# Performance work log

Measured on AMD Instinct MI355X. Metric: run time of the kernel, lower is better.

Reference implementation:

```python
import jax, jax.numpy as jnp
import numpy as np

B, D, F = 16384, 512, 28
GIN = D + D + F + 1  # 1053
EPS = 1e-5


def setup_inputs() -> dict:
    key = jax.random.key(0)
    ks = jax.random.split(key, 16)
    s = 0.02
    return {
        "team_embedding": jax.random.normal(ks[0], (B, D), jnp.float32),
        "opponent_embedding": jax.random.normal(ks[1], (B, D), jnp.float32),
        "game_features": jax.random.normal(ks[2], (B, F), jnp.float32),
        "won": jnp.round(jax.random.uniform(ks[3], (B, 1), jnp.float32)),
        # input_projection Linear(GIN -> D)
        "W_proj": jax.random.normal(ks[4], (D, GIN), jnp.float32) * s,
        "b_proj": jnp.zeros((D,), jnp.float32),
        # GRUCell params (PyTorch layout: [3D, *] with r,z,n blocks)
        "W_ih": jax.random.normal(ks[5], (3 * D, D), jnp.float32) * s,
        "b_ih": jnp.zeros((3 * D,), jnp.float32),
        "W_hh": jax.random.normal(ks[6], (3 * D, D), jnp.float32) * s,
        "b_hh": jnp.zeros((3 * D,), jnp.float32),
        # LayerNorm
        "gamma": jnp.ones((D,), jnp.float32),
        "beta": jnp.zeros((D,), jnp.float32),
        # game_importance MLP: D -> 128 -> 1
        "W_imp1": jax.random.normal(ks[7], (128, D), jnp.float32) * s,
        "b_imp1": jnp.zeros((128,), jnp.float32),
        "W_imp2": jax.random.normal(ks[8], (1, 128), jnp.float32) * s,
        "b_imp2": jnp.zeros((1,), jnp.float32),
    }


def reference(team_embedding, opponent_embedding, game_features, won,
              W_proj, b_proj, W_ih, b_ih, W_hh, b_hh,
              gamma, beta, W_imp1, b_imp1, W_imp2, b_imp2):
    # combined: [B, 2D+F+1]
    x = jnp.concatenate([team_embedding, opponent_embedding, game_features, won], axis=-1)
    # input_projection: Linear -> ReLU (Dropout is identity in eval)
    projected = jax.nn.relu(x @ W_proj.T + b_proj)  # [B, D]
    # game_importance: Linear -> ReLU -> Linear -> Sigmoid
    importance = jax.nn.sigmoid(jax.nn.relu(projected @ W_imp1.T + b_imp1) @ W_imp2.T + b_imp2)  # [B, 1]
    # GRUCell (PyTorch math)
    gi = projected @ W_ih.T + b_ih          # [B, 3D]
    gh = team_embedding @ W_hh.T + b_hh     # [B, 3D]
    i_r, i_z, i_n = jnp.split(gi, 3, axis=-1)
    h_r, h_z, h_n = jnp.split(gh, 3, axis=-1)
    r = jax.nn.sigmoid(i_r + h_r)
    z = jax.nn.sigmoid(i_z + h_z)
    n = jnp.tanh(i_n + r * h_n)
    new_embedding = (1.0 - z) * n + z * team_embedding
    # gated blend
    updated = team_embedding + importance * (new_embedding - team_embedding)
    # LayerNorm
    mu = jnp.mean(updated, axis=-1, keepdims=True)
    var = jnp.mean(jnp.square(updated - mu), axis=-1, keepdims=True)
    updated = gamma * (updated - mu) * jax.lax.rsqrt(var + EPS) + beta
    game_context = jax.lax.stop_gradient(projected)  # .detach().clone()
    return (updated, game_context)
```

## Files before the change

kernel.cpp:

```cpp
#include <hip/hip_runtime.h>
#include <hip/hip_bf16.h>


#define NB 16384
#define GINP 1088

typedef __bf16 bf16x8 __attribute__((ext_vector_type(8)));
typedef float f32x4 __attribute__((ext_vector_type(4)));
typedef unsigned short ushort8 __attribute__((ext_vector_type(8)));

__device__ __forceinline__ void gload_lds16(const void* g, void* l) {
  __builtin_amdgcn_global_load_lds(
      (const __attribute__((address_space(1))) void*)g,
      (__attribute__((address_space(3))) void*)l, 16, 0, 0);
}
__device__ __forceinline__ bf16x8 ds_read128(const unsigned short* l) {
  f32x4 r;
  asm volatile("ds_read_b128 %0, %1"
               : "=v"(r)
               : "v"((const __attribute__((address_space(3))) void*)l));
  bf16x8 out;
  __builtin_memcpy(&out, &r, 16);
  return out;
}
__device__ __forceinline__ float sigmoidf_(float x) { return 1.0f / (1.0f + expf(-x)); }
__device__ __forceinline__ float bf2f(unsigned short u) {
  unsigned int x = ((unsigned int)u) << 16;
  float f; __builtin_memcpy(&f, &x, 4); return f;
}

__global__ __launch_bounds__(256) void prep_x2(
    const float* __restrict__ team, const float* __restrict__ opp,
    const float* __restrict__ gf, const float* __restrict__ won,
    __hip_bfloat16* __restrict__ X) {
  long idx = (long)blockIdx.x * 256 + threadIdx.x;
  if (idx >= (long)NB * 136) return;
  const int r = (int)(idx / 136);
  const int c8 = (int)(idx % 136) * 8;
  float v[8];
  if (c8 < 512) {
    float4 a = *(const float4*)&team[(size_t)r * 512 + c8];
    float4 b = *(const float4*)&team[(size_t)r * 512 + c8 + 4];
    v[0]=a.x; v[1]=a.y; v[2]=a.z; v[3]=a.w; v[4]=b.x; v[5]=b.y; v[6]=b.z; v[7]=b.w;
  } else if (c8 < 1024) {
    float4 a = *(const float4*)&opp[(size_t)r * 512 + (c8 - 512)];
    float4 b = *(const float4*)&opp[(size_t)r * 512 + (c8 - 512) + 4];
    v[0]=a.x; v[1]=a.y; v[2]=a.z; v[3]=a.w; v[4]=b.x; v[5]=b.y; v[6]=b.z; v[7]=b.w;
  } else if (c8 < 1048) {
    const int g0 = c8 - 1024;
#pragma unroll
    for (int e = 0; e < 8; ++e) v[e] = gf[(size_t)r * 28 + g0 + e];
  } else if (c8 == 1048) {
    v[0] = gf[(size_t)r * 28 + 24]; v[1] = gf[(size_t)r * 28 + 25];
    v[2] = gf[(size_t)r * 28 + 26]; v[3] = gf[(size_t)r * 28 + 27];
    v[4] = won[r]; v[5] = 0.f; v[6] = 0.f; v[7] = 0.f;
  } else {
#pragma unroll
    for (int e = 0; e < 8; ++e) v[e] = 0.f;
  }
  __hip_bfloat16 h[8];
#pragma unroll
  for (int e = 0; e < 8; ++e) h[e] = __float2bfloat16(v[e]);
  *(uint4*)&X[(size_t)r * GINP + c8] = *(const uint4*)h;
}

__global__ __launch_bounds__(256) void prep_w2(
    const float* __restrict__ Wproj, const float* __restrict__ Wih,
    const float* __restrict__ Whh, const float* __restrict__ Wimp1,
    const float* __restrict__ bih, const float* __restrict__ bhh,
    __hip_bfloat16* __restrict__ Wpb, __hip_bfloat16* __restrict__ Wrz,
    __hip_bfloat16* __restrict__ Wn, __hip_bfloat16* __restrict__ Wimp1b,
    float* __restrict__ bcat) {
  long idx = (long)blockIdx.x * 256 + threadIdx.x;
  if (idx < 512L * 1088) {
    int r = (int)(idx / 1088), c = (int)(idx % 1088);
    Wpb[idx] = __float2bfloat16(c < 1053 ? Wproj[(size_t)r * 1053 + c] : 0.f);
    return;
  }
  idx -= 512L * 1088;
  if (idx < 1024L * 1024) {
    int q = (int)(idx >> 10), c = (int)(idx & 1023);
    float v = (c < 512) ? Wih[(size_t)q * 512 + c] : Whh[(size_t)q * 512 + (c - 512)];
    Wrz[idx] = __float2bfloat16(v);
    return;
  }
  idx -= 1024L * 1024;
  if (idx < 1024L * 512) {
    int q = (int)(idx / 512), c = (int)(idx % 512);
    float v = (q < 512) ? Wih[(size_t)(1024 + q) * 512 + c]
                        : Whh[(size_t)(1024 + q - 512) * 512 + c];
    Wn[idx] = __float2bfloat16(v);
    return;
  }
  idx -= 1024L * 512;
  if (idx < 128L * 512) { Wimp1b[idx] = __float2bfloat16(Wimp1[idx]); return; }
  idx -= 128L * 512;
  if (idx < 2048) {
    int j = (int)idx;
    float v;
    if (j < 1024) v = bih[j] + bhh[j];
    else if (j < 1536) v = bih[j];
    else v = bhh[j - 512];
    bcat[j] = v;
  }
}

__global__ __launch_bounds__(512, 1) void gemm_g8(
    const __hip_bfloat16* __restrict__ Pm, const __hip_bfloat16* __restrict__ Xb,
    const __hip_bfloat16* __restrict__ Wrz, const __hip_bfloat16* __restrict__ Wn,
    const float* __restrict__ bcat, __hip_bfloat16* __restrict__ gg) {
  __shared__ __align__(16) unsigned short ldsA[2 * 256 * 64];
  __shared__ __align__(16) unsigned short ldsB[2 * 256 * 64];

  const int tid = threadIdx.x;
  const int wid = tid >> 6, lane = tid & 63;
  const int wr = wid >> 2, wc = wid & 3;
  const int fl = lane & 15, kh = lane >> 4;
  const int srow = tid >> 3;
  const int sgp = tid & 7;

  const int tn = blockIdx.x & 7, tm = blockIdx.x >> 3;
  const int m0 = tm * 256;

  const __hip_bfloat16* Wp;
  int ldw, NT;
  if (tn < 4) { Wp = Wrz + (size_t)tn * 256 * 1024; ldw = 1024; NT = 16; }
  else        { Wp = Wn + (size_t)(tn - 4) * 256 * 512; ldw = 512; NT = 8; }
  const float* bp = bcat + tn * 256;

  auto stageA64 = [&](int s, int r0) {
    const __hip_bfloat16* Ap; int lda; int k0;
    if (tn < 4) {
      if (s < 8) { Ap = Pm; lda = 512; k0 = s * 64; }
      else       { Ap = Xb; lda = GINP; k0 = (s - 8) * 64; }
    } else if (tn < 6) { Ap = Pm; lda = 512; k0 = s * 64; }
    else               { Ap = Xb; lda = GINP; k0 = s * 64; }
    const int row = r0 + srow;
    const int gl = sgp ^ (row & 7);
    gload_lds16(Ap + (size_t)(m0 + row) * lda + k0 + gl * 8,
                &ldsA[(s & 1) * 16384 + (r0 + (wid << 3)) * 64]);
  };
  auto stageB64 = [&](int s, int r0) {
    const int row = r0 + srow;
    const int gl = sgp ^ (row & 7);
    gload_lds16(Wp + (size_t)row * ldw + s * 64 + gl * 8,
                &ldsB[(s & 1) * 16384 + (r0 + (wid << 3)) * 64]);
  };
  auto readA = [&](int sl, int m, int kk) -> bf16x8 {
    const int row = wr * 128 + m * 16 + fl;
    const int g = (kk * 4 + kh) ^ (row & 7);
    return ds_read128(&ldsA[sl + row * 64 + g * 8]);
  };
  auto readB = [&](int sl, int n, int kk) -> bf16x8 {
    const int row = wc * 64 + n * 16 + fl;
    const int g = (kk * 4 + kh) ^ (row & 7);
    return ds_read128(&ldsB[sl + row * 64 + g * 8]);
  };

  f32x4 acc[8][4];
#pragma unroll
  for (int m = 0; m < 8; ++m)
#pragma unroll
    for (int n = 0; n < 4; ++n) acc[m][n] = (f32x4){0.f, 0.f, 0.f, 0.f};

  stageA64(0, 0); stageA64(0, 64); stageA64(0, 128); stageA64(0, 192);
  stageB64(0, 0); stageB64(0, 64); stageB64(0, 128); stageB64(0, 192);
  stageA64(1, 0); stageA64(1, 64); stageA64(1, 128); stageA64(1, 192);
  stageB64(1, 0); stageB64(1, 64); stageB64(1, 128); stageB64(1, 192);
  asm volatile("s_waitcnt vmcnt(8)" ::: "memory");
  __builtin_amdgcn_s_barrier();

  for (int t = 0; t < NT; ++t) {
    const int sl = (t & 1) * 16384;
    const bool pf = (t + 2 < NT);
    bf16x8 fa0[4][2], fa1[4][2], fb0[2][2], fb1[2][2];

#pragma unroll
    for (int m = 0; m < 4; ++m) { fa0[m][0] = readA(sl, m, 0); fa0[m][1] = readA(sl, m, 1); }
#pragma unroll
    for (int n = 0; n < 2; ++n) { fb0[n][0] = readB(sl, n, 0); fb0[n][1] = readB(sl, n, 1); }
    __builtin_amdgcn_s_barrier();
    asm volatile("s_waitcnt lgkmcnt(0)" ::: "memory");
    __builtin_amdgcn_sched_barrier(0);
    __builtin_amdgcn_s_setprio(1);
#pragma unroll
    for (int kk = 0; kk < 2; ++kk)
#pragma unroll
      for (int m = 0; m < 4; ++m)
#pragma unroll
        for (int n = 0; n < 2; ++n)
          acc[m][n] = __builtin_amdgcn_mfma_f32_16x16x32_bf16(fa0[m][kk], fb0[n][kk], acc[m][n], 0, 0, 0);
    __builtin_amdgcn_s_setprio(0);
    __builtin_amdgcn_s_barrier();

#pragma unroll
    for (int m = 0; m < 4; ++m) { fa1[m][0] = readA(sl, m + 4, 0); fa1[m][1] = readA(sl, m + 4, 1); }
    if (pf) { stageA64(t + 2, 0); stageA64(t + 2, 128); }
    __builtin_amdgcn_s_barrier();
    asm volatile("s_waitcnt lgkmcnt(0)" ::: "memory");
    __builtin_amdgcn_sched_barrier(0);
    __builtin_amdgcn_s_setprio(1);
#pragma unroll
    for (int kk = 0; kk < 2; ++kk)
#pragma unroll
      for (int m = 0; m < 4; ++m)
#pragma unroll
        for (int n = 0; n < 2; ++n)
          acc[m + 4][n] = __builtin_amdgcn_mfma_f32_16x16x32_bf16(fa1[m][kk], fb0[n][kk], acc[m + 4][n], 0, 0, 0);
    __builtin_amdgcn_s_setprio(0);
    __builtin_amdgcn_s_barrier();

#pragma unroll
    for (int n = 0; n < 2; ++n) { fb1[n][0] = readB(sl, n + 2, 0); fb1[n][1] = readB(sl, n + 2, 1); }
    if (pf) { stageA64(t + 2, 64); stageA64(t + 2, 192); }
    __builtin_amdgcn_s_barrier();
    asm volatile("s_waitcnt lgkmcnt(0)" ::: "memory");
    __builtin_amdgcn_sched_barrier(0);
    __builtin_amdgcn_s_setprio(1);
#pragma unroll
    for (int kk = 0; kk < 2; ++kk)
#pragma unroll
      for (int m = 0; m < 4; ++m)
#pragma unroll
        for (int n = 0; n < 2; ++n)
          acc[m + 4][n + 2] = __builtin_amdgcn_mfma_f32_16x16x32_bf16(fa1[m][kk], fb1[n][kk], acc[m + 4][n + 2], 0, 0, 0);
    __builtin_amdgcn_s_setprio(0);
    __builtin_amdgcn_s_barrier();

    if (pf) { stageB64(t + 2, 0); stageB64(t + 2, 64); stageB64(t + 2, 128); stageB64(t + 2, 192); }
    __builtin_amdgcn_sched_barrier(0);
    __builtin_amdgcn_s_barrier();
    __builtin_amdgcn_s_setprio(1);
#pragma unroll
    for (int kk = 0; kk < 2; ++kk)
#pragma unroll
      for (int m = 0; m < 4; ++m)
#pragma unroll
        for (int n = 0; n < 2; ++n)
          acc[m][n + 2] = __builtin_amdgcn_mfma_f32_16x16x32_bf16(fa0[m][kk], fb1[n][kk], acc[m][n + 2], 0, 0, 0);
    __builtin_amdgcn_s_setprio(0);
    if (pf) { asm volatile("s_waitcnt vmcnt(8)" ::: "memory"); }
    else    { asm volatile("s_waitcnt vmcnt(0)" ::: "memory"); }
    __builtin_amdgcn_s_barrier();
  }

#pragma unroll
  for (int m = 0; m < 8; ++m)
#pragma unroll
    for (int n = 0; n < 4; ++n)
#pragma unroll
      for (int j = 0; j < 4; ++j) {
        const int lrow = wr * 128 + m * 16 + kh * 4 + j;
        const int lcol = wc * 64 + n * 16 + fl;
        gg[(size_t)(m0 + lrow) * 2048 + tn * 256 + lcol] =
            __float2bfloat16(acc[m][n][j] + bp[lcol]);
      }
}

template <int MODE>
__global__ __launch_bounds__(512, 1) void gemm_dp3(
    const __hip_bfloat16* __restrict__ A0, int lda0,
    const __hip_bfloat16* __restrict__ A1, int lda1,
    const __hip_bfloat16* __restrict__ W0, const __hip_bfloat16* __restrict__ W1,
    const float* __restrict__ bias,
    float* __restrict__ Cf, __hip_bfloat16* __restrict__ Cb,
    int tilesN, int NTP) {
  __shared__ __align__(16) unsigned short ldsA[3 * 256 * 64];
  __shared__ __align__(16) unsigned short ldsB[3 * 128 * 64];

  const int tid = threadIdx.x;
  const int wid = tid >> 6, lane = tid & 63;
  const int wr = wid >> 1, wc = wid & 1;
  const int fl = lane & 15, kh = lane >> 4;

  int bid = blockIdx.x;
  { const int cpx = gridDim.x >> 3; bid = (bid & 7) * cpx + (bid >> 3); }
  const int tm = bid / tilesN, tn = bid % tilesN;
  const int m0 = tm * 256;

  const __hip_bfloat16* Wp; int ldw, NT;
  Wp = W0 + (size_t)tn * 128 * GINP; ldw = GINP; NT = NTP;
  const float* bp = bias + tn * 128;

  const int prow_b = tid >> 3;
  const int gp = tid & 7;

  auto stageAB = [&](int s, int buf) {
    const int kW = s * 64;
    const __hip_bfloat16* Ap = A0; int lda = lda0; int kA = s * 64;
    unsigned short* la = &ldsA[buf * (256 * 64)];
    unsigned short* lb = &ldsB[buf * (128 * 64)];
#pragma unroll
    for (int i = 0; i < 4; ++i) {
      const int prow = i * 64 + prow_b;
      const int gl = gp ^ (prow & 7);
      gload_lds16(Ap + (size_t)(m0 + prow) * lda + kA + gl * 8,
                  la + i * 4096 + wid * 512);
    }
#pragma unroll
    for (int i = 0; i < 2; ++i) {
      const int prow = i * 64 + prow_b;
      const int gl = gp ^ (prow & 7);
      gload_lds16(Wp + (size_t)prow * ldw + kW + gl * 8,
                  lb + i * 4096 + wid * 512);
    }
  };

  f32x4 acc[4][4];
#pragma unroll
  for (int m = 0; m < 4; ++m)
#pragma unroll
    for (int n = 0; n < 4; ++n) acc[m][n] = (f32x4){0.f, 0.f, 0.f, 0.f};

  stageAB(0, 0);
  stageAB(1, 1);

  for (int t = 0; t < NT; ++t) {
    const int cur = t % 3;
    if (t + 1 < NT) { asm volatile("s_waitcnt vmcnt(6)" ::: "memory"); }
    else            { asm volatile("s_waitcnt vmcnt(0)" ::: "memory"); }
    __builtin_amdgcn_s_barrier();
    if (t + 2 < NT) stageAB(t + 2, (t + 2) % 3);

    const unsigned short* At = &ldsA[cur * (256 * 64)];
    const unsigned short* Bt = &ldsB[cur * (128 * 64)];
    bf16x8 af[2][4], bfr[2][4];
#pragma unroll
    for (int kk = 0; kk < 2; ++kk) {
#pragma unroll
      for (int m = 0; m < 4; ++m) {
        const int r = wr * 64 + m * 16 + fl;
        const int g = (kk * 4 + kh) ^ (r & 7);
        af[kk][m] = ds_read128(&At[r * 64 + g * 8]);
      }
#pragma unroll
      for (int n = 0; n < 4; ++n) {
        const int r = wc * 64 + n * 16 + fl;
        const int g = (kk * 4 + kh) ^ (r & 7);
        bfr[kk][n] = ds_read128(&Bt[r * 64 + g * 8]);
      }
    }
    asm volatile("s_waitcnt lgkmcnt(0)" ::: "memory");
    __builtin_amdgcn_sched_barrier(0);
    __builtin_amdgcn_s_setprio(1);
#pragma unroll
    for (int kk = 0; kk < 2; ++kk)
#pragma unroll
      for (int m = 0; m < 4; ++m)
#pragma unroll
        for (int n = 0; n < 4; ++n)
          acc[m][n] = __builtin_amdgcn_mfma_f32_16x16x32_bf16(af[kk][m], bfr[kk][n], acc[m][n], 0, 0, 0);
    __builtin_amdgcn_s_setprio(0);
  }

#pragma unroll
  for (int m = 0; m < 4; ++m)
#pragma unroll
    for (int n = 0; n < 4; ++n)
#pragma unroll
      for (int j = 0; j < 4; ++j) {
        const int lrow = wr * 64 + m * 16 + kh * 4 + j;
        const int lcol = wc * 64 + n * 16 + fl;
        const size_t grow = (size_t)(m0 + lrow);
        float v = acc[m][n][j] + bp[lcol];
        v = fmaxf(v, 0.f);
        Cf[grow * 512 + tn * 128 + lcol] = v;
        Cb[grow * 512 + tn * 128 + lcol] = __float2bfloat16(v);
      }
}

__global__ __launch_bounds__(256, 2) void gemm_imp2(
    const __hip_bfloat16* __restrict__ A, const __hip_bfloat16* __restrict__ W,
    const float* __restrict__ bias, const float* __restrict__ w2,
    const float* __restrict__ b2, float* __restrict__ imp) {
  __shared__ __align__(16) unsigned short ldsA[64 * 64];
  __shared__ __align__(16) unsigned short ldsB[128 * 64];
  __shared__ float sdot[64];
  const int tid = threadIdx.x;
  const int w = tid >> 6, lane = tid & 63;
  const int wr = w >> 1, wc = w & 1;
  const int fl = lane & 15, kh = lane >> 4;
  const int srow = lane >> 3, scol = (lane & 7) * 8;
  const int m0 = blockIdx.x * 64;

  if (tid < 64) sdot[tid] = 0.f;

  f32x4 acc[2][4];
#pragma unroll
  for (int m = 0; m < 2; ++m)
#pragma unroll
    for (int n = 0; n < 4; ++n) acc[m][n] = (f32x4){0.f, 0.f, 0.f, 0.f};

  for (int kt = 0; kt < 8; ++kt) {
    const int k0 = kt * 64;
#pragma unroll
    for (int c = 0; c < 2; ++c) {
      const int rgrp = c * 4 + w;
      const int row = rgrp * 8 + srow;
      gload_lds16(A + (size_t)(m0 + row) * 512 + k0 + scol, (char*)ldsA + rgrp * 1024);
    }
#pragma unroll
    for (int c = 0; c < 4; ++c) {
      const int rgrp = c * 4 + w;
      const int row = rgrp * 8 + srow;
      gload_lds16(W + (size_t)row * 512 + k0 + scol, (char*)ldsB + rgrp * 1024);
    }
    __syncthreads();
#pragma unroll
    for (int kk = 0; kk < 2; ++kk) {
      bf16x8 af[2], bfr[4];
#pragma unroll
      for (int m = 0; m < 2; ++m)
        af[m] = *(const bf16x8*)&ldsA[(wr * 32 + m * 16 + fl) * 64 + kk * 32 + kh * 8];
#pragma unroll
      for (int n = 0; n < 4; ++n)
        bfr[n] = *(const bf16x8*)&ldsB[(wc * 64 + n * 16 + fl) * 64 + kk * 32 + kh * 8];
#pragma unroll
      for (int m = 0; m < 2; ++m)
#pragma unroll
        for (int n = 0; n < 4; ++n)
          acc[m][n] = __builtin_amdgcn_mfma_f32_16x16x32_bf16(af[m], bfr[n], acc[m][n], 0, 0, 0);
    }
    __syncthreads();
  }
#pragma unroll
  for (int m = 0; m < 2; ++m)
#pragma unroll
    for (int j = 0; j < 4; ++j) {
      float p = 0.f;
#pragma unroll
      for (int n = 0; n < 4; ++n) {
        const int lcol = wc * 64 + n * 16 + fl;
        const float v = fmaxf(acc[m][n][j] + bias[lcol], 0.f);
        p += v * w2[lcol];
      }
      atomicAdd(&sdot[wr * 32 + m * 16 + kh * 4 + j], p);
    }
  __syncthreads();
  if (tid < 64) imp[m0 + tid] = sigmoidf_(sdot[tid] + b2[0]);
}

__global__ __launch_bounds__(256) void fuse_final2(
    const float* __restrict__ team, const __hip_bfloat16* __restrict__ gg,
    const float* __restrict__ imp, const float* __restrict__ gamma,
    const float* __restrict__ beta, float* __restrict__ out) {
  const int row = blockIdx.x * 4 + (threadIdx.x >> 6);
  const int lane = threadIdx.x & 63;
  const size_t gb = (size_t)row * 2048 + lane * 8;
  ushort8 sr = *(const ushort8*)&gg[gb];
  ushort8 szv = *(const ushort8*)&gg[gb + 512];
  ushort8 inn = *(const ushort8*)&gg[gb + 1024];
  ushort8 hnn = *(const ushort8*)&gg[gb + 1536];
  float4 t0 = *(const float4*)&team[(size_t)row * 512 + lane * 8];
  float4 t1 = *(const float4*)&team[(size_t)row * 512 + lane * 8 + 4];
  const float im = imp[row];
  float tv[8] = {t0.x, t0.y, t0.z, t0.w, t1.x, t1.y, t1.z, t1.w};
  float u[8];
  float s = 0.f, ss = 0.f;
#pragma unroll
  for (int e = 0; e < 8; ++e) {
    const float rg = sigmoidf_(bf2f(sr[e]));
    const float zg = sigmoidf_(bf2f(szv[e]));
    const float ng = tanhf(bf2f(inn[e]) + rg * bf2f(hnn[e]));
    const float ne = (1.f - zg) * ng + zg * tv[e];
    const float uu = tv[e] + im * (ne - tv[e]);
    u[e] = uu; s += uu; ss += uu * uu;
  }
#pragma unroll
  for (int off = 32; off; off >>= 1) {
    s += __shfl_down(s, off);
    ss += __shfl_down(ss, off);
  }
  s = __shfl(s, 0); ss = __shfl(ss, 0);
  const float mu = s * (1.f / 512.f);
  const float inv = rsqrtf(ss * (1.f / 512.f) - mu * mu + 1e-5f);
  float4 g0 = *(const float4*)&gamma[lane * 8], g1 = *(const float4*)&gamma[lane * 8 + 4];
  float4 b0 = *(const float4*)&beta[lane * 8], b1 = *(const float4*)&beta[lane * 8 + 4];
  float gv[8] = {g0.x, g0.y, g0.z, g0.w, g1.x, g1.y, g1.z, g1.w};
  float bv[8] = {b0.x, b0.y, b0.z, b0.w, b1.x, b1.y, b1.z, b1.w};
  float4 o0, o1;
  o0.x = gv[0] * (u[0] - mu) * inv + bv[0];
  o0.y = gv[1] * (u[1] - mu) * inv + bv[1];
  o0.z = gv[2] * (u[2] - mu) * inv + bv[2];
  o0.w = gv[3] * (u[3] - mu) * inv + bv[3];
  o1.x = gv[4] * (u[4] - mu) * inv + bv[4];
  o1.y = gv[5] * (u[5] - mu) * inv + bv[5];
  o1.z = gv[6] * (u[6] - mu) * inv + bv[6];
  o1.w = gv[7] * (u[7] - mu) * inv + bv[7];
  *(float4*)&out[(size_t)row * 512 + lane * 8] = o0;
  *(float4*)&out[(size_t)row * 512 + lane * 8 + 4] = o1;
}

extern "C" void kernel_launch(void* const* d_in, const int* in_sizes, int n_in,
                              void* d_out, int out_size, void* d_ws, size_t ws_size,
                              hipStream_t stream) {
  const float* team   = (const float*)d_in[0];
  const float* opp    = (const float*)d_in[1];
  const float* gf     = (const float*)d_in[2];
  const float* won    = (const float*)d_in[3];
  const float* W_proj = (const float*)d_in[4];
  const float* b_proj = (const float*)d_in[5];
  const float* W_ih   = (const float*)d_in[6];
  const float* b_ih   = (const float*)d_in[7];
  const float* W_hh   = (const float*)d_in[8];
  const float* b_hh   = (const float*)d_in[9];
  const float* gamma  = (const float*)d_in[10];
  const float* beta   = (const float*)d_in[11];
  const float* W_imp1 = (const float*)d_in[12];
  const float* b_imp1 = (const float*)d_in[13];
  const float* W_imp2 = (const float*)d_in[14];
  const float* b_imp2 = (const float*)d_in[15];

  char* ws = (char*)d_ws;
  size_t o = 0;
  __hip_bfloat16* Xbf    = (__hip_bfloat16*)(ws + o); o += (size_t)NB * GINP * 2;
  __hip_bfloat16* Wpb    = (__hip_bfloat16*)(ws + o); o += (size_t)512 * GINP * 2;
  __hip_bfloat16* Wrz    = (__hip_bfloat16*)(ws + o); o += (size_t)1024 * 1024 * 2;
  __hip_bfloat16* Wn     = (__hip_bfloat16*)(ws + o); o += (size_t)1024 * 512 * 2;
  __hip_bfloat16* Wimp1b = (__hip_bfloat16*)(ws + o); o += (size_t)128 * 512 * 2;
  float*          bcat   = (float*)(ws + o);          o += (size_t)2048 * 4;
  __hip_bfloat16* Pbf    = (__hip_bfloat16*)(ws + o); o += (size_t)NB * 512 * 2;
  float*          imp    = (float*)(ws + o);          o += (size_t)NB * 4;
  __hip_bfloat16* gg     = (__hip_bfloat16*)(ws + o); o += (size_t)NB * 2048 * 2;

  float* out_updated = (float*)d_out;
  float* out_ctx     = (float*)d_out + (size_t)NB * 512;

  prep_x2<<<(NB * 136 + 255) / 256, 256, 0, stream>>>(team, opp, gf, won, Xbf);
  {
    const long total = 512L * 1088 + 1024L * 1024 + 1024L * 512 + 128L * 512 + 2048;
    prep_w2<<<(int)((total + 255) / 256), 256, 0, stream>>>(
        W_proj, W_ih, W_hh, W_imp1, b_ih, b_hh, Wpb, Wrz, Wn, Wimp1b, bcat);
  }
  gemm_dp3<0><<<256, 512, 0, stream>>>(Xbf, GINP, nullptr, 0, Wpb, nullptr, b_proj,
                                       out_ctx, Pbf, 4, 17);
  gemm_imp2<<<NB / 64, 256, 0, stream>>>(Pbf, Wimp1b, b_imp1, W_imp2, b_imp2, imp);
  gemm_g8<<<512, 512, 0, stream>>>(Pbf, Xbf, Wrz, Wn, bcat, gg);
  fuse_final2<<<NB / 4, 256, 0, stream>>>(team, gg, imp, gamma, beta, out_updated);
}
```

Before: 169.8 us.

## Merge prep kernels and simplify gate GEMM to single-stage prefetch loop

Fuses the activation and weight bf16 conversion kernels into one launch, removing a kernel boundary. The gate GEMM's hand-interleaved 8-phase schedule is replaced by a simpler loop. Each iteration prefetches tile t+1 into the other LDS buffer, then reads fragments and issues MFMAs in two k-halves. This trades fine-grained overlap of loads and MFMAs for fewer barriers and less code, so memory latency may be less well hidden.

```diff
diff --git a/kernel.cpp b/kernel.cpp
--- a/kernel.cpp
+++ b/kernel.cpp
@@ -29,49 +29,50 @@
   float f; __builtin_memcpy(&f, &x, 4); return f;
 }
 
-__global__ __launch_bounds__(256) void prep_x2(
+#define PREP_X_BLOCKS ((NB * 136 + 255) / 256)
+__global__ __launch_bounds__(256) void prep_all(
     const float* __restrict__ team, const float* __restrict__ opp,
     const float* __restrict__ gf, const float* __restrict__ won,
-    __hip_bfloat16* __restrict__ X) {
-  long idx = (long)blockIdx.x * 256 + threadIdx.x;
-  if (idx >= (long)NB * 136) return;
-  const int r = (int)(idx / 136);
-  const int c8 = (int)(idx % 136) * 8;
-  float v[8];
-  if (c8 < 512) {
-    float4 a = *(const float4*)&team[(size_t)r * 512 + c8];
-    float4 b = *(const float4*)&team[(size_t)r * 512 + c8 + 4];
-    v[0]=a.x; v[1]=a.y; v[2]=a.z; v[3]=a.w; v[4]=b.x; v[5]=b.y; v[6]=b.z; v[7]=b.w;
-  } else if (c8 < 1024) {
-    float4 a = *(const float4*)&opp[(size_t)r * 512 + (c8 - 512)];
-    float4 b = *(const float4*)&opp[(size_t)r * 512 + (c8 - 512) + 4];
-    v[0]=a.x; v[1]=a.y; v[2]=a.z; v[3]=a.w; v[4]=b.x; v[5]=b.y; v[6]=b.z; v[7]=b.w;
-  } else if (c8 < 1048) {
-    const int g0 = c8 - 1024;
-#pragma unroll
-    for (int e = 0; e < 8; ++e) v[e] = gf[(size_t)r * 28 + g0 + e];
-  } else if (c8 == 1048) {
-    v[0] = gf[(size_t)r * 28 + 24]; v[1] = gf[(size_t)r * 28 + 25];
-    v[2] = gf[(size_t)r * 28 + 26]; v[3] = gf[(size_t)r * 28 + 27];
-    v[4] = won[r]; v[5] = 0.f; v[6] = 0.f; v[7] = 0.f;
-  } else {
-#pragma unroll
-    for (int e = 0; e < 8; ++e) v[e] = 0.f;
-  }
-  __hip_bfloat16 h[8];
-#pragma unroll
-  for (int e = 0; e < 8; ++e) h[e] = __float2bfloat16(v[e]);
-  *(uint4*)&X[(size_t)r * GINP + c8] = *(const uint4*)h;
-}
-
-__global__ __launch_bounds__(256) void prep_w2(
     const float* __restrict__ Wproj, const float* __restrict__ Wih,
     const float* __restrict__ Whh, const float* __restrict__ Wimp1,
     const float* __restrict__ bih, const float* __restrict__ bhh,
+    __hip_bfloat16* __restrict__ X,
     __hip_bfloat16* __restrict__ Wpb, __hip_bfloat16* __restrict__ Wrz,
     __hip_bfloat16* __restrict__ Wn, __hip_bfloat16* __restrict__ Wimp1b,
     float* __restrict__ bcat) {
-  long idx = (long)blockIdx.x * 256 + threadIdx.x;
+  if (blockIdx.x < PREP_X_BLOCKS) {
+    long idx = (long)blockIdx.x * 256 + threadIdx.x;
+    if (idx >= (long)NB * 136) return;
+    const int r = (int)(idx / 136);
+    const int c8 = (int)(idx % 136) * 8;
+    float v[8];
+    if (c8 < 512) {
+      float4 a = *(const float4*)&team[(size_t)r * 512 + c8];
+      float4 b = *(const float4*)&team[(size_t)r * 512 + c8 + 4];
+      v[0]=a.x; v[1]=a.y; v[2]=a.z; v[3]=a.w; v[4]=b.x; v[5]=b.y; v[6]=b.z; v[7]=b.w;
+    } else if (c8 < 1024) {
+      float4 a = *(const float4*)&opp[(size_t)r * 512 + (c8 - 512)];
+      float4 b = *(const float4*)&opp[(size_t)r * 512 + (c8 - 512) + 4];
+      v[0]=a.x; v[1]=a.y; v[2]=a.z; v[3]=a.w; v[4]=b.x; v[5]=b.y; v[6]=b.z; v[7]=b.w;
+    } else if (c8 < 1048) {
+      const int g0 = c8 - 1024;
+#pragma unroll
+      for (int e = 0; e < 8; ++e) v[e] = gf[(size_t)r * 28 + g0 + e];
+    } else if (c8 == 1048) {
+      v[0] = gf[(size_t)r * 28 + 24]; v[1] = gf[(size_t)r * 28 + 25];
+      v[2] = gf[(size_t)r * 28 + 26]; v[3] = gf[(size_t)r * 28 + 27];
+      v[4] = won[r]; v[5] = 0.f; v[6] = 0.f; v[7] = 0.f;
+    } else {
+#pragma unroll
+      for (int e = 0; e < 8; ++e) v[e] = 0.f;
+    }
+    __hip_bfloat16 h[8];
+#pragma unroll
+    for (int e = 0; e < 8; ++e) h[e] = __float2bfloat16(v[e]);
+    *(uint4*)&X[(size_t)r * GINP + c8] = *(const uint4*)h;
+    return;
+  }
+  long idx = (long)(blockIdx.x - PREP_X_BLOCKS) * 256 + threadIdx.x;
   if (idx < 512L * 1088) {
     int r = (int)(idx / 1088), c = (int)(idx % 1088);
     Wpb[idx] = __float2bfloat16(c < 1053 ? Wproj[(size_t)r * 1053 + c] : 0.f);
@@ -105,7 +106,7 @@
   }
 }
 
-__global__ __launch_bounds__(512, 1) void gemm_g8(
+__global__ __launch_bounds__(512, 1) void gemm_g2(
     const __hip_bfloat16* __restrict__ Pm, const __hip_bfloat16* __restrict__ Xb,
     const __hip_bfloat16* __restrict__ Wrz, const __hip_bfloat16* __restrict__ Wn,
     const float* __restrict__ bcat, __hip_bfloat16* __restrict__ gg) {
@@ -165,83 +166,51 @@
 
   stageA64(0, 0); stageA64(0, 64); stageA64(0, 128); stageA64(0, 192);
   stageB64(0, 0); stageB64(0, 64); stageB64(0, 128); stageB64(0, 192);
-  stageA64(1, 0); stageA64(1, 64); stageA64(1, 128); stageA64(1, 192);
-  stageB64(1, 0); stageB64(1, 64); stageB64(1, 128); stageB64(1, 192);
-  asm volatile("s_waitcnt vmcnt(8)" ::: "memory");
-  __builtin_amdgcn_s_barrier();
 
   for (int t = 0; t < NT; ++t) {
     const int sl = (t & 1) * 16384;
-    const bool pf = (t + 2 < NT);
-    bf16x8 fa0[4][2], fa1[4][2], fb0[2][2], fb1[2][2];
-
-#pragma unroll
-    for (int m = 0; m < 4; ++m) { fa0[m][0] = readA(sl, m, 0); fa0[m][1] = readA(sl, m, 1); }
-#pragma unroll
-    for (int n = 0; n < 2; ++n) { fb0[n][0] = readB(sl, n, 0); fb0[n][1] = readB(sl, n, 1); }
     __builtin_amdgcn_s_barrier();
-    asm volatile("s_waitcnt lgkmcnt(0)" ::: "memory");
-    __builtin_amdgcn_sched_barrier(0);
-    __builtin_amdgcn_s_setprio(1);
-#pragma unroll
-    for (int kk = 0; kk < 2; ++kk)
-#pragma unroll
-      for (int m = 0; m < 4; ++m)
-#pragma unroll
-        for (int n = 0; n < 2; ++n)
-          acc[m][n] = __builtin_amdgcn_mfma_f32_16x16x32_bf16(fa0[m][kk], fb0[n][kk], acc[m][n], 0, 0, 0);
-    __builtin_amdgcn_s_setprio(0);
+    if (t + 1 < NT) {
+      stageA64(t + 1, 0); stageA64(t + 1, 64); stageA64(t + 1, 128); stageA64(t + 1, 192);
+      stageB64(t + 1, 0); stageB64(t + 1, 64); stageB64(t + 1, 128); stageB64(t + 1, 192);
+      asm volatile("s_waitcnt vmcnt(8)" ::: "memory");
+    } else {
+      asm volatile("s_waitcnt vmcnt(0)" ::: "memory");
+    }
     __builtin_amdgcn_s_barrier();
 
-#pragma unroll
-    for (int m = 0; m < 4; ++m) { fa1[m][0] = readA(sl, m + 4, 0); fa1[m][1] = readA(sl, m + 4, 1); }
-    if (pf) { stageA64(t + 2, 0); stageA64(t + 2, 128); }
-    __builtin_amdgcn_s_barrier();
-    asm volatile("s_waitcnt lgkmcnt(0)" ::: "memory");
-    __builtin_amdgcn_sched_barrier(0);
-    __builtin_amdgcn_s_setprio(1);
-#pragma unroll
-    for (int kk = 0; kk < 2; ++kk)
-#pragma unroll
-      for (int m = 0; m < 4; ++m)
-#pragma unroll
-        for (int n = 0; n < 2; ++n)
-          acc[m + 4][n] = __builtin_amdgcn_mfma_f32_16x16x32_bf16(fa1[m][kk], fb0[n][kk], acc[m + 4][n], 0, 0, 0);
-    __builtin_amdgcn_s_setprio(0);
-    __builtin_amdgcn_s_barrier();
-
-#pragma unroll
-    for (int n = 0; n < 2; ++n) { fb1[n][0] = readB(sl, n + 2, 0); fb1[n][1] = readB(sl, n + 2, 1); }
-    if (pf) { stageA64(t + 2, 64); stageA64(t + 2, 192); }
-    __builtin_amdgcn_s_barrier();
-    asm volatile("s_waitcnt lgkmcnt(0)" ::: "memory");
-    __builtin_amdgcn_sched_barrier(0);
-    __builtin_amdgcn_s_setprio(1);
-#pragma unroll
-    for (int kk = 0; kk < 2; ++kk)
-#pragma unroll
-      for (int m = 0; m < 4; ++m)
-#pragma unroll
-        for (int n = 0; n < 2; ++n)
-          acc[m + 4][n + 2] = __builtin_amdgcn_mfma_f32_16x16x32_bf16(fa1[m][kk], fb1[n][kk], acc[m + 4][n + 2], 0, 0, 0);
-    __builtin_amdgcn_s_setprio(0);
-    __builtin_amdgcn_s_barrier();
-
-    if (pf) { stageB64(t + 2, 0); stageB64(t + 2, 64); stageB64(t + 2, 128); stageB64(t + 2, 192); }
-    __builtin_amdgcn_sched_barrier(0);
-    __builtin_amdgcn_s_barrier();
-    __builtin_amdgcn_s_setprio(1);
-#pragma unroll
-    for (int kk = 0; kk < 2; ++kk)
-#pragma unroll
-      for (int m = 0; m < 4; ++m)
-#pragma unroll
-        for (int n = 0; n < 2; ++n)
-          acc[m][n + 2] = __builtin_amdgcn_mfma_f32_16x16x32_bf16(fa0[m][kk], fb1[n][kk], acc[m][n + 2], 0, 0, 0);
-    __builtin_amdgcn_s_setprio(0);
-    if (pf) { asm volatile("s_waitcnt vmcnt(8)" ::: "memory"); }
-    else    { asm volatile("s_waitcnt vmcnt(0)" ::: "memory"); }
-    __builtin_amdgcn_s_barrier();
+    {
+      bf16x8 a0[8], b0[4];
+#pragma unroll
+      for (int m = 0; m < 8; ++m) a0[m] = readA(sl, m, 0);
+#pragma unroll
+      for (int n = 0; n < 4; ++n) b0[n] = readB(sl, n, 0);
+      asm volatile("s_waitcnt lgkmcnt(0)" ::: "memory");
+      __builtin_amdgcn_sched_barrier(0);
+      __builtin_amdgcn_s_setprio(1);
+#pragma unroll
+      for (int m = 0; m < 8; ++m)
+#pragma unroll
+        for (int n = 0; n < 4; ++n)
+          acc[m][n] = __builtin_amdgcn_mfma_f32_16x16x32_bf16(a0[m], b0[n], acc[m][n], 0, 0, 0);
+      __builtin_amdgcn_s_setprio(0);
+    }
+    {
+      bf16x8 a1[8], b1[4];
+#pragma unroll
+      for (int m = 0; m < 8; ++m) a1[m] = readA(sl, m, 1);
+#pragma unroll
+      for (int n = 0; n < 4; ++n) b1[n] = readB(sl, n, 1);
+      asm volatile("s_waitcnt lgkmcnt(0)" ::: "memory");
+      __builtin_amdgcn_sched_barrier(0);
+      __builtin_amdgcn_s_setprio(1);
+#pragma unroll
+      for (int m = 0; m < 8; ++m)
+#pragma unroll
+        for (int n = 0; n < 4; ++n)
+          acc[m][n] = __builtin_amdgcn_mfma_f32_16x16x32_bf16(a1[m], b1[n], acc[m][n], 0, 0, 0);
+      __builtin_amdgcn_s_setprio(0);
+    }
   }
 
 #pragma unroll
@@ -257,12 +226,9 @@
       }
 }
 
-template <int MODE>
 __global__ __launch_bounds__(512, 1) void gemm_dp3(
     const __hip_bfloat16* __restrict__ A0, int lda0,
-    const __hip_bfloat16* __restrict__ A1, int lda1,
-    const __hip_bfloat16* __restrict__ W0, const __hip_bfloat16* __restrict__ W1,
-    const float* __restrict__ bias,
+    const __hip_bfloat16* __restrict__ W0, const float* __restrict__ bias,
     float* __restrict__ Cf, __hip_bfloat16* __restrict__ Cb,
     int tilesN, int NTP) {
   __shared__ __align__(16) unsigned short ldsA[3 * 256 * 64];
@@ -278,8 +244,8 @@
   const int tm = bid / tilesN, tn = bid % tilesN;
   const int m0 = tm * 256;
 
-  const __hip_bfloat16* Wp; int ldw, NT;
-  Wp = W0 + (size_t)tn * 128 * GINP; ldw = GINP; NT = NTP;
+  const __hip_bfloat16* Wp = W0 + (size_t)tn * 128 * GINP;
+  const int ldw = GINP, NT = NTP;
   const float* bp = bias + tn * 128;
 
   const int prow_b = tid >> 3;
@@ -526,15 +492,15 @@
   float* out_updated = (float*)d_out;
   float* out_ctx     = (float*)d_out + (size_t)NB * 512;
 
-  prep_x2<<<(NB * 136 + 255) / 256, 256, 0, stream>>>(team, opp, gf, won, Xbf);
   {
-    const long total = 512L * 1088 + 1024L * 1024 + 1024L * 512 + 128L * 512 + 2048;
-    prep_w2<<<(int)((total + 255) / 256), 256, 0, stream>>>(
-        W_proj, W_ih, W_hh, W_imp1, b_ih, b_hh, Wpb, Wrz, Wn, Wimp1b, bcat);
-  }
-  gemm_dp3<0><<<256, 512, 0, stream>>>(Xbf, GINP, nullptr, 0, Wpb, nullptr, b_proj,
-                                       out_ctx, Pbf, 4, 17);
+    const long wtotal = 512L * 1088 + 1024L * 1024 + 1024L * 512 + 128L * 512 + 2048;
+    const int wblocks = (int)((wtotal + 255) / 256);
+    prep_all<<<PREP_X_BLOCKS + wblocks, 256, 0, stream>>>(
+        team, opp, gf, won, W_proj, W_ih, W_hh, W_imp1, b_ih, b_hh,
+        Xbf, Wpb, Wrz, Wn, Wimp1b, bcat);
+  }
+  gemm_dp3<<<256, 512, 0, stream>>>(Xbf, GINP, Wpb, b_proj, out_ctx, Pbf, 4, 17);
   gemm_imp2<<<NB / 64, 256, 0, stream>>>(Pbf, Wimp1b, b_imp1, W_imp2, b_imp2, imp);
-  gemm_g8<<<512, 512, 0, stream>>>(Pbf, Xbf, Wrz, Wn, bcat, gg);
+  gemm_g2<<<512, 512, 0, stream>>>(Pbf, Xbf, Wrz, Wn, bcat, gg);
   fuse_final2<<<NB / 4, 256, 0, stream>>>(team, gg, imp, gamma, beta, out_updated);
 }
```

After: 164.0 us. -3.4%, faster.
